# Kernel optimization log

Hardware: AMD Instinct MI355X
Metric: run time of the kernel (lower is better)

The kernel has to match this reference:

```python
import jax, jax.numpy as jnp
import numpy as np

N_EMBD = 768
NUM_EXPERTS = 64
EXPERT_WIDTH = 256            # all experts uniform width (expert_sizes=[(64,256)])
TOTAL_WIDTH = NUM_EXPERTS * EXPERT_WIDTH  # 16384
TOP_K = 8


def setup_inputs() -> dict:
    key = jax.random.key(0)
    k1, k2, k3, k4 = jax.random.split(key, 4)
    B, S = 1, 2048
    x = jax.random.normal(k1, (B, S, N_EMBD), dtype=jnp.float32)
    # router: nn.Linear(n_embd, num_experts, bias=False) -> weight [E, n_embd]
    router_w = jax.random.normal(k2, (NUM_EXPERTS, N_EMBD), dtype=jnp.float32) * 0.02
    # trunc_normal(std=0.02) approximated by clipped normal
    w1 = jnp.clip(jax.random.normal(k3, (N_EMBD, TOTAL_WIDTH), dtype=jnp.float32) * 0.02, -0.06, 0.06)
    w2 = jnp.clip(jax.random.normal(k4, (TOTAL_WIDTH, N_EMBD), dtype=jnp.float32) * 0.02, -0.06, 0.06)
    return {"x": x, "router_w": router_w, "w1": w1, "w2": w2}


def reference(x, router_w, w1, w2):
    B, S, D = x.shape
    T = B * S
    x_flat = x.reshape(T, D)

    # Router: sigmoid gating + top-k
    router_logits = x_flat @ router_w.T                      # [T, E]
    router_probs = jax.nn.sigmoid(router_logits.astype(jnp.float32))
    top_k_weights, selected_experts = jax.lax.top_k(router_probs, TOP_K)  # [T, K]
    top_k_weights = top_k_weights / (top_k_weights.sum(axis=-1, keepdims=True) + 1e-20)
    top_k_weights = top_k_weights.astype(x.dtype)

    # Per-token expert combine weights [T, E]: 0 for unselected experts.
    tok_idx = jnp.arange(T)[:, None]
    w_tok = jnp.zeros((T, NUM_EXPERTS), dtype=x.dtype).at[tok_idx, selected_experts].set(top_k_weights)

    # Expert MLP (relu^2 activation), dense-masked equivalent of
    # padded_gather -> grouped GEMM -> padded_scatter.
    h = jnp.square(jax.nn.relu(x_flat @ w1))                 # [T, E*W]
    h = (h.reshape(T, NUM_EXPERTS, EXPERT_WIDTH) * w_tok[:, :, None]).reshape(T, TOTAL_WIDTH)
    output = (h @ w2).reshape(B, S, D)

    # Aux losses
    router_z_loss = jnp.mean(jnp.square(jax.nn.logsumexp(router_logits, axis=-1)))
    tokens_per_expert = jnp.zeros((NUM_EXPERTS,), dtype=jnp.float32).at[selected_experts.reshape(-1)].add(1.0)
    f_i = (tokens_per_expert / tokens_per_expert.sum()).astype(x.dtype)
    p_i = router_probs.mean(axis=0)
    # all expert widths equal -> num_experts * (f_i . p_i)
    load_balance_loss = NUM_EXPERTS * (f_i.astype(jnp.float32) @ p_i)
    # expert_widths_normalized == ones -> mean over tokens of sum of probs
    compute_loss = router_probs.sum(axis=-1).mean()

    return output, router_z_loss, load_balance_loss, compute_loss, f_i
```

## Files before the change

### kernel.cpp

```cpp
#include <hip/hip_runtime.h>
#include <hip/hip_bf16.h>

#define T_TOKENS 2048
#define D_EMBD 768
#define N_EXP 64
#define EW 256
#define TOPK 8
#define TW (N_EXP*EW)
#define PAD_SLOTS 20480
#define SCHED_MAX 2560
#define OUT_BASE (2048*768)

typedef __attribute__((ext_vector_type(8))) short bf16x8;
typedef __attribute__((ext_vector_type(4))) float f32x4;

typedef __attribute__((address_space(1))) void GAS;
typedef __attribute__((address_space(3))) void LAS;
#define GLOAD16(g, l) __builtin_amdgcn_global_load_lds((GAS*)(g), (LAS*)(l), 16, 0, 0)

__device__ inline unsigned short f2bu(float f) {
  union { __hip_bfloat16 b; unsigned short u; } cv; cv.b = __float2bfloat16(f); return cv.u;
}
__device__ inline unsigned int pk2(float a, float b) {
  return (unsigned int)f2bu(a) | ((unsigned int)f2bu(b) << 16);
}

__global__ void k_init(int* counts, int* cursor, float* psum, float* scal,
                       float* wgt_slot, int* tok_slot, int* sched_e) {
  int i = blockIdx.x*256 + threadIdx.x;
  if (i < N_EXP) { counts[i] = 0; cursor[i] = 0; psum[i] = 0.f; }
  if (i < 2) scal[i] = 0.f;
  if (i < PAD_SLOTS) { wgt_slot[i] = 0.f; tok_slot[i] = 0; }
  if (i < SCHED_MAX) sched_e[i] = -1;
}

__global__ __launch_bounds__(256) void k_logits(const float* __restrict__ x,
                                                const float* __restrict__ rw,
                                                float* __restrict__ lp) {
  __shared__ float rw_s[8][256];
  int tid = threadIdx.x;
  int tg = blockIdx.x, eg = blockIdx.y, kc = blockIdx.z;
  #pragma unroll
  for (int idx = 0; idx < 8; idx++)
    rw_s[idx][tid] = rw[(size_t)(eg*8 + idx)*D_EMBD + kc*256 + tid];
  __syncthreads();
  int tok = tg*256 + tid;
  const float4* x4 = reinterpret_cast<const float4*>(x + (size_t)tok*D_EMBD + kc*256);
  float acc[8];
  #pragma unroll
  for (int e = 0; e < 8; e++) acc[e] = 0.f;
  #pragma unroll 4
  for (int k4 = 0; k4 < 64; k4++) {
    float4 xv = x4[k4];
    #pragma unroll
    for (int e = 0; e < 8; e++)
      acc[e] += xv.x*rw_s[e][k4*4+0] + xv.y*rw_s[e][k4*4+1]
              + xv.z*rw_s[e][k4*4+2] + xv.w*rw_s[e][k4*4+3];
  }
  float* dst = lp + (size_t)kc*T_TOKENS*N_EXP + (size_t)tok*N_EXP + eg*8;
  float4 o0 = {acc[0], acc[1], acc[2], acc[3]};
  float4 o1 = {acc[4], acc[5], acc[6], acc[7]};
  reinterpret_cast<float4*>(dst)[0] = o0;
  reinterpret_cast<float4*>(dst)[1] = o1;
}

__global__ __launch_bounds__(256) void k_router2(const float* __restrict__ lp,
                          int* __restrict__ sel_e, float* __restrict__ sel_w,
                          int* __restrict__ counts, float* __restrict__ psum,
                          float* __restrict__ scal) {
  __shared__ float psum_s[4][64];
  __shared__ int cnt_s[4][64];
  int tid = threadIdx.x, wv = tid >> 6, lane = tid & 63;
  float pacc = 0.f, zacc = 0.f;
  int cacc = 0;
  int tbase = blockIdx.x*8 + wv*2;
  #pragma unroll
  for (int it = 0; it < 2; it++) {
    int t = tbase + it;
    float logit = lp[(size_t)t*N_EXP + lane]
                + lp[(size_t)T_TOKENS*N_EXP + (size_t)t*N_EXP + lane]
                + lp[2*(size_t)T_TOKENS*N_EXP + (size_t)t*N_EXP + lane];
    float prob = 1.f/(1.f + expf(-logit));
    pacc += prob;
    float mx = logit;
    for (int s = 32; s; s >>= 1) mx = fmaxf(mx, __shfl_xor(mx, s, 64));
    float sse = expf(logit - mx);
    for (int s = 32; s; s >>= 1) sse += __shfl_xor(sse, s, 64);
    float lse = mx + logf(sse);
    zacc += lse*lse;
    int rank = 0;
    #pragma unroll
    for (int j = 0; j < 64; j++) {
      float pj = __shfl(prob, j, 64);
      rank += (pj > prob || (pj == prob && j < lane)) ? 1 : 0;
    }
    bool sel = rank < TOPK;
    float sp = sel ? prob : 0.f;
    for (int s = 32; s; s >>= 1) sp += __shfl_xor(sp, s, 64);
    if (sel) {
      sel_e[t*TOPK + rank] = lane;
      sel_w[t*TOPK + rank] = prob / (sp + 1e-20f);
      cacc++;
    }
  }
  psum_s[wv][lane] = pacc;
  cnt_s[wv][lane] = cacc;
  if (lane == 0) atomicAdd(&scal[0], zacc);
  __syncthreads();
  if (tid < 64) {
    float p = psum_s[0][tid] + psum_s[1][tid] + psum_s[2][tid] + psum_s[3][tid];
    int c = cnt_s[0][tid] + cnt_s[1][tid] + cnt_s[2][tid] + cnt_s[3][tid];
    atomicAdd(&psum[tid], p);
    atomicAdd(&counts[tid], c);
  }
}

__global__ void k_schedule(const int* __restrict__ counts, int* __restrict__ offsets,
                           int* __restrict__ sched_e, int* __restrict__ sched_r0) {
  int e = threadIdx.x;
  int c = counts[e];
  int tiles = (c + 63) >> 6;
  int padded = tiles << 6;
  int ip = padded;
  for (int s = 1; s < 64; s <<= 1) { int v = __shfl_up(ip, s, 64); if (e >= s) ip += v; }
  int rowoff = ip - padded;
  offsets[e] = rowoff;
  int it = tiles;
  for (int s = 8; s < 64; s <<= 1) { int v = __shfl_up(it, s, 64); if (e >= s) it += v; }
  int rank = it - tiles;
  int xcd = e & 7;
  for (int i = 0; i < tiles; i++) {
    int p = xcd + 8*(rank + i);
    sched_e[p] = e;
    sched_r0[p] = rowoff + i*64;
  }
}

__global__ void k_assign(const int* __restrict__ sel_e, const float* __restrict__ sel_w,
                         const int* __restrict__ offsets, int* __restrict__ cursor,
                         int* __restrict__ tok_slot, float* __restrict__ wgt_slot,
                         int* __restrict__ slot_tk) {
  int i = blockIdx.x*256 + threadIdx.x;
  int e = sel_e[i];
  int pos = atomicAdd(&cursor[e], 1);
  int slot = offsets[e] + pos;
  tok_slot[slot] = i >> 3;
  wgt_slot[slot] = sel_w[i];
  slot_tk[i] = slot;
}

template<int MODE>
__global__ __launch_bounds__(256) void k_moe_gemm(
    const void* __restrict__ Asrc, const float* __restrict__ Bsrc,
    const int* __restrict__ sched_e, const int* __restrict__ sched_r0,
    const int* __restrict__ tok_slot, const float* __restrict__ wgt_slot,
    __hip_bfloat16* __restrict__ outp) {
  constexpr int NS   = (MODE == 1) ? 12 : 4;
  constexpr int BSTR = (MODE == 1) ? TW : D_EMBD;
  __shared__ __hip_bfloat16 As[2][64*64];
  __shared__ __hip_bfloat16 Bs[2][128*64];
  int tid = threadIdx.x;
  int nch = blockIdx.y;
  int n4 = tid & 31, kpb = tid >> 5;
  int mrow = tid >> 4, k4f = tid & 15;
  int arl = tid >> 3, akc = tid & 7;
  int a_off = ((akc ^ (arl & 7)) << 3);
  int wv = tid >> 6, lane = tid & 63;
  int wm = wv >> 1, wn = wv & 1;
  int l15 = lane & 15, l4 = lane >> 4;

  for (int p = blockIdx.x; p < SCHED_MAX; p += gridDim.x) {
    int e = sched_e[p];
    if (e < 0) continue;
    int r0 = sched_r0[p];

    int browb = (MODE == 1) ? 0 : e*EW;
    int bcolb = (MODE == 1) ? (e*EW + nch*128) : nch*128;

    int tks[4];
    size_t a_base0 = 0, a_base1 = 0;
    if (MODE == 1) {
      #pragma unroll
      for (int i = 0; i < 4; i++) tks[i] = tok_slot[r0 + i*16 + mrow];
    } else {
      a_base0 = (size_t)(r0 + arl) * EW;
      a_base1 = (size_t)(r0 + arl + 32) * EW;
    }

    float bv[8][4], av[4][4];

    auto B_LOAD = [&](int k0) {
      const float* rp = Bsrc + (size_t)(browb + k0 + kpb*8)*BSTR + bcolb + n4*4;
      #pragma unroll
      for (int r = 0; r < 8; r++)
        *reinterpret_cast<float4*>(&bv[r][0]) =
            *reinterpret_cast<const float4*>(rp + (size_t)r*BSTR);
    };
    auto B_WRITE = [&](int bsel) {
      char* bs = (char*)&Bs[bsel][0];
      #pragma unroll
      for (int c = 0; c < 4; c++) {
        int n = n4*4 + c;
        int ch = kpb ^ ((n & 7) ^ ((n >> 3) & 7));
        uint4 o = { pk2(bv[0][c], bv[1][c]), pk2(bv[2][c], bv[3][c]),
                    pk2(bv[4][c], bv[5][c]), pk2(bv[6][c], bv[7][c]) };
        *reinterpret_cast<uint4*>(bs + n*128 + ch*16) = o;
      }
    };
    auto A_LOAD1 = [&](int k0) {
      const float* xf = (const float*)Asrc;
      #pragma unroll
      for (int i = 0; i < 4; i++)
        *reinterpret_cast<float4*>(&av[i][0]) =
            *reinterpret_cast<const float4*>(xf + (size_t)tks[i]*D_EMBD + k0 + k4f*4);
    };
    auto A_WRITE1 = [&](int bsel) {
      char* as_ = (char*)&As[bsel][0];
      #pragma unroll
      for (int i = 0; i < 4; i++) {
        int m = i*16 + mrow;
        int ch = (k4f >> 1) ^ (m & 7);
        uint2 val = { pk2(av[i][0], av[i][1]), pk2(av[i][2], av[i][3]) };
        *reinterpret_cast<uint2*>(as_ + m*128 + ch*16 + (k4f & 1)*8) = val;
      }
    };
    auto A_GLOAD2 = [&](int bsel, int k0) {
      const __hip_bfloat16* hb = (const __hip_bfloat16*)Asrc;
      GLOAD16(hb + a_base0 + k0 + a_off, &As[bsel][0] + tid*8);
      GLOAD16(hb + a_base1 + k0 + a_off, &As[bsel][0] + (256 + tid)*8);
    };

    f32x4 acc[2][4];
    f32x4 z = {0.f, 0.f, 0.f, 0.f};
    #pragma unroll
    for (int m = 0; m < 2; m++)
      #pragma unroll
      for (int n = 0; n < 4; n++) acc[m][n] = z;

    if (MODE == 1) { A_LOAD1(0); B_LOAD(0); A_WRITE1(0); B_WRITE(0); }
    else           { A_GLOAD2(0, 0); B_LOAD(0); B_WRITE(0);
                     asm volatile("s_waitcnt vmcnt(0)" ::: "memory"); }
    __syncthreads();

    int cur = 0;
    for (int step = 0; step < NS; step++) {
      bool more = (step + 1 < NS);
      int k1 = (step + 1)*64;
      if (more) {
        if (MODE == 1) { A_LOAD1(k1); B_LOAD(k1); }
        else           { A_GLOAD2(cur ^ 1, k1); B_LOAD(k1); }
      }
      const char* asC = (const char*)&As[cur][0];
      const char* bsC = (const char*)&Bs[cur][0];
      bf16x8 af[2][2], bq[4][2];
      #pragma unroll
      for (int m = 0; m < 2; m++) {
        int ra = wm*32 + m*16 + l15;
        #pragma unroll
        for (int kk = 0; kk < 2; kk++)
          af[m][kk] = *reinterpret_cast<const bf16x8*>(
              asC + ra*128 + (((kk*4 + l4) ^ (ra & 7)) << 4));
      }
      #pragma unroll
      for (int n = 0; n < 4; n++) {
        int rb = wn*64 + n*16 + l15;
        int Sb = (rb & 7) ^ ((rb >> 3) & 7);
        #pragma unroll
        for (int kk = 0; kk < 2; kk++)
          bq[n][kk] = *reinterpret_cast<const bf16x8*>(
              bsC + rb*128 + (((kk*4 + l4) ^ Sb) << 4));
      }
      #pragma unroll
      for (int kk = 0; kk < 2; kk++)
        #pragma unroll
        for (int m = 0; m < 2; m++)
          #pragma unroll
          for (int n = 0; n < 4; n++)
            acc[m][n] = __builtin_amdgcn_mfma_f32_16x16x32_bf16(af[m][kk], bq[n][kk], acc[m][n], 0, 0, 0);
      if (more) {
        if (MODE == 1) { A_WRITE1(cur ^ 1); B_WRITE(cur ^ 1); }
        else           { B_WRITE(cur ^ 1);
                         asm volatile("s_waitcnt vmcnt(0)" ::: "memory"); }
      }
      __syncthreads();
      cur ^= 1;
    }

    if (MODE == 1) {
      #pragma unroll
      for (int m = 0; m < 2; m++)
        #pragma unroll
        for (int j = 0; j < 4; j++) {
          int r = r0 + wm*32 + m*16 + l4*4 + j;
          float wg = wgt_slot[r];
          #pragma unroll
          for (int n = 0; n < 4; n++) {
            int col = nch*128 + wn*64 + n*16 + l15;
            float v = fmaxf(acc[m][n][j], 0.f);
            outp[(size_t)r*EW + col] = __float2bfloat16(v*v*wg);
          }
        }
    } else {
      #pragma unroll
      for (int m = 0; m < 2; m++)
        #pragma unroll
        for (int j = 0; j < 4; j++) {
          int r = r0 + wm*32 + m*16 + l4*4 + j;
          #pragma unroll
          for (int n = 0; n < 4; n++) {
            int col = nch*128 + wn*64 + n*16 + l15;
            outp[(size_t)r*D_EMBD + col] = __float2bfloat16(acc[m][n][j]);
          }
        }
    }
  }
}

__global__ void k_combine(const __hip_bfloat16* __restrict__ y, const int* __restrict__ slot_tk,
                          float* __restrict__ out) {
  __shared__ int s[TOPK];
  int t = blockIdx.x, tid = threadIdx.x;
  if (tid < TOPK) s[tid] = slot_tk[t*TOPK + tid];
  __syncthreads();
  if (tid < 192) {
    int c = tid*4;
    float a0 = 0.f, a1 = 0.f, a2 = 0.f, a3 = 0.f;
    #pragma unroll
    for (int k = 0; k < TOPK; k++) {
      ushort4 v = *reinterpret_cast<const ushort4*>(&y[(size_t)s[k]*D_EMBD + c]);
      union { unsigned int u; float f; } f0, f1, f2, f3;
      f0.u = ((unsigned int)v.x) << 16;
      f1.u = ((unsigned int)v.y) << 16;
      f2.u = ((unsigned int)v.z) << 16;
      f3.u = ((unsigned int)v.w) << 16;
      a0 += f0.f; a1 += f1.f; a2 += f2.f; a3 += f3.f;
    }
    float4 o = {a0, a1, a2, a3};
    *reinterpret_cast<float4*>(&out[(size_t)t*D_EMBD + c]) = o;
  }
}

__global__ void k_finalize(const int* __restrict__ counts, const float* __restrict__ psum,
                           const float* __restrict__ scal, float* __restrict__ out) {
  __shared__ float part[N_EXP], ptot[N_EXP];
  int e = threadIdx.x;
  float f = (float)counts[e] / 16384.f;
  float p = psum[e] / 2048.f;
  part[e] = f * p;
  ptot[e] = p;
  out[OUT_BASE + 3 + e] = f;
  __syncthreads();
  if (e == 0) {
    float s = 0.f, q = 0.f;
    for (int i = 0; i < N_EXP; i++) { s += part[i]; q += ptot[i]; }
    out[OUT_BASE + 0] = scal[0] / 2048.f;
    out[OUT_BASE + 1] = 64.f * s;
    out[OUT_BASE + 2] = q;
  }
}

extern "C" void kernel_launch(void* const* d_in, const int* in_sizes, int n_in,
                              void* d_out, int out_size, void* d_ws, size_t ws_size,
                              hipStream_t stream) {
  const float* x  = (const float*)d_in[0];
  const float* rw = (const float*)d_in[1];
  const float* w1 = (const float*)d_in[2];
  const float* w2 = (const float*)d_in[3];
  float* out = (float*)d_out;
  char* ws = (char*)d_ws;

  size_t o = 0;
  auto alloc = [&](size_t b) { size_t r = o; o += (b + 255) & ~(size_t)255; return r; };
  __hip_bfloat16* hprm  = (__hip_bfloat16*)(ws + alloc((size_t)PAD_SLOTS*256*2));
  __hip_bfloat16* yprm  = (__hip_bfloat16*)(ws + alloc((size_t)PAD_SLOTS*768*2));
  float* lp      = (float*)(ws + alloc(3UL*2048*64*4));
  int*   sel_e   = (int*)  (ws + alloc(16384UL*4));
  float* sel_w   = (float*)(ws + alloc(16384UL*4));
  int*   slot_tk = (int*)  (ws + alloc(16384UL*4));
  int*   tokslot = (int*)  (ws + alloc((size_t)PAD_SLOTS*4));
  float* wgtslot = (float*)(ws + alloc((size_t)PAD_SLOTS*4));
  int*   counts  = (int*)  (ws + alloc(256));
  int*   cursor  = (int*)  (ws + alloc(256));
  float* psum    = (float*)(ws + alloc(256));
  float* scal    = (float*)(ws + alloc(256));
  int*   offsets = (int*)  (ws + alloc(256));
  int*   sch_e   = (int*)  (ws + alloc(SCHED_MAX*4));
  int*   sch_r0  = (int*)  (ws + alloc(SCHED_MAX*4));

  k_init<<<80, 256, 0, stream>>>(counts, cursor, psum, scal, wgtslot, tokslot, sch_e);
  k_logits<<<dim3(8, 8, 3), 256, 0, stream>>>(x, rw, lp);
  k_router2<<<256, 256, 0, stream>>>(lp, sel_e, sel_w, counts, psum, scal);
  k_schedule<<<1, 64, 0, stream>>>(counts, offsets, sch_e, sch_r0);
  k_assign<<<64, 256, 0, stream>>>(sel_e, sel_w, offsets, cursor, tokslot, wgtslot, slot_tk);
  k_moe_gemm<1><<<dim3(512, 2), 256, 0, stream>>>((const void*)x, w1, sch_e, sch_r0, tokslot, wgtslot, hprm);
  k_moe_gemm<2><<<dim3(512, 6), 256, 0, stream>>>((const void*)hprm, w2, sch_e, sch_r0, tokslot, wgtslot, yprm);
  k_combine<<<2048, 256, 0, stream>>>(yprm, slot_tk, out);
  k_finalize<<<1, 64, 0, stream>>>(counts, psum, scal, out);
}
```

Before: 141.7 us.

## Fuse expert up- and down-projection GEMMs into one kernel with LDS-resident hidden tile

Merges the two MoE GEMM kernels into one. Each block computes the 64x256 relu²-weighted hidden tile for its row group into shared memory, then immediately multiplies it by the expert's w2 slice for all six output column chunks. This removes the bf16 hidden buffer round-trip through global memory and one kernel launch. In exchange, per-block parallelism drops from 8 blocks per schedule entry (2+6 via grid y) to one block doing all the work. LDS use also grows by 32KB, which lowers occupancy and serializes the work inside each block.

```diff
diff --git a/kernel.cpp b/kernel.cpp
--- a/kernel.cpp
+++ b/kernel.cpp
@@ -13,10 +13,6 @@
 
 typedef __attribute__((ext_vector_type(8))) short bf16x8;
 typedef __attribute__((ext_vector_type(4))) float f32x4;
-
-typedef __attribute__((address_space(1))) void GAS;
-typedef __attribute__((address_space(3))) void LAS;
-#define GLOAD16(g, l) __builtin_amdgcn_global_load_lds((GAS*)(g), (LAS*)(l), 16, 0, 0)
 
 __device__ inline unsigned short f2bu(float f) {
   union { __hip_bfloat16 b; unsigned short u; } cv; cv.b = __float2bfloat16(f); return cv.u;
@@ -149,22 +145,18 @@
   slot_tk[i] = slot;
 }
 
-template<int MODE>
-__global__ __launch_bounds__(256) void k_moe_gemm(
-    const void* __restrict__ Asrc, const float* __restrict__ Bsrc,
+__global__ __launch_bounds__(256) void k_moe_mlp(
+    const float* __restrict__ x, const float* __restrict__ w1,
+    const float* __restrict__ w2,
     const int* __restrict__ sched_e, const int* __restrict__ sched_r0,
     const int* __restrict__ tok_slot, const float* __restrict__ wgt_slot,
-    __hip_bfloat16* __restrict__ outp) {
-  constexpr int NS   = (MODE == 1) ? 12 : 4;
-  constexpr int BSTR = (MODE == 1) ? TW : D_EMBD;
+    __hip_bfloat16* __restrict__ yprm) {
   __shared__ __hip_bfloat16 As[2][64*64];
   __shared__ __hip_bfloat16 Bs[2][128*64];
+  __shared__ __hip_bfloat16 Hs[64*256];
   int tid = threadIdx.x;
-  int nch = blockIdx.y;
   int n4 = tid & 31, kpb = tid >> 5;
   int mrow = tid >> 4, k4f = tid & 15;
-  int arl = tid >> 3, akc = tid & 7;
-  int a_off = ((akc ^ (arl & 7)) << 3);
   int wv = tid >> 6, lane = tid & 63;
   int wm = wv >> 1, wn = wv & 1;
   int l15 = lane & 15, l4 = lane >> 4;
@@ -174,29 +166,27 @@
     if (e < 0) continue;
     int r0 = sched_r0[p];
 
-    int browb = (MODE == 1) ? 0 : e*EW;
-    int bcolb = (MODE == 1) ? (e*EW + nch*128) : nch*128;
-
     int tks[4];
-    size_t a_base0 = 0, a_base1 = 0;
-    if (MODE == 1) {
-      #pragma unroll
-      for (int i = 0; i < 4; i++) tks[i] = tok_slot[r0 + i*16 + mrow];
-    } else {
-      a_base0 = (size_t)(r0 + arl) * EW;
-      a_base1 = (size_t)(r0 + arl + 32) * EW;
-    }
+    #pragma unroll
+    for (int i = 0; i < 4; i++) tks[i] = tok_slot[r0 + i*16 + mrow];
+
+    const float* bsrc = w1;
+    int bstr = TW;
+    size_t browb = 0;
+    int bcolb = 0;
 
     float bv[8][4], av[4][4];
-
-    auto B_LOAD = [&](int k0) {
-      const float* rp = Bsrc + (size_t)(browb + k0 + kpb*8)*BSTR + bcolb + n4*4;
+    f32x4 acc[2][4];
+    f32x4 z = {0.f, 0.f, 0.f, 0.f};
+
+    auto B_LD = [&](int k0) {
+      const float* rp = bsrc + (browb + (size_t)(k0 + kpb*8))*bstr + bcolb + n4*4;
       #pragma unroll
       for (int r = 0; r < 8; r++)
         *reinterpret_cast<float4*>(&bv[r][0]) =
-            *reinterpret_cast<const float4*>(rp + (size_t)r*BSTR);
-    };
-    auto B_WRITE = [&](int bsel) {
+            *reinterpret_cast<const float4*>(rp + (size_t)r*bstr);
+    };
+    auto B_WR = [&](int bsel) {
       char* bs = (char*)&Bs[bsel][0];
       #pragma unroll
       for (int c = 0; c < 4; c++) {
@@ -207,14 +197,13 @@
         *reinterpret_cast<uint4*>(bs + n*128 + ch*16) = o;
       }
     };
-    auto A_LOAD1 = [&](int k0) {
-      const float* xf = (const float*)Asrc;
+    auto A_LD = [&](int k0) {
       #pragma unroll
       for (int i = 0; i < 4; i++)
         *reinterpret_cast<float4*>(&av[i][0]) =
-            *reinterpret_cast<const float4*>(xf + (size_t)tks[i]*D_EMBD + k0 + k4f*4);
-    };
-    auto A_WRITE1 = [&](int bsel) {
+            *reinterpret_cast<const float4*>(x + (size_t)tks[i]*D_EMBD + k0 + k4f*4);
+    };
+    auto A_WR = [&](int bsel) {
       char* as_ = (char*)&As[bsel][0];
       #pragma unroll
       for (int i = 0; i < 4; i++) {
@@ -224,43 +213,14 @@
         *reinterpret_cast<uint2*>(as_ + m*128 + ch*16 + (k4f & 1)*8) = val;
       }
     };
-    auto A_GLOAD2 = [&](int bsel, int k0) {
-      const __hip_bfloat16* hb = (const __hip_bfloat16*)Asrc;
-      GLOAD16(hb + a_base0 + k0 + a_off, &As[bsel][0] + tid*8);
-      GLOAD16(hb + a_base1 + k0 + a_off, &As[bsel][0] + (256 + tid)*8);
-    };
-
-    f32x4 acc[2][4];
-    f32x4 z = {0.f, 0.f, 0.f, 0.f};
-    #pragma unroll
-    for (int m = 0; m < 2; m++)
-      #pragma unroll
-      for (int n = 0; n < 4; n++) acc[m][n] = z;
-
-    if (MODE == 1) { A_LOAD1(0); B_LOAD(0); A_WRITE1(0); B_WRITE(0); }
-    else           { A_GLOAD2(0, 0); B_LOAD(0); B_WRITE(0);
-                     asm volatile("s_waitcnt vmcnt(0)" ::: "memory"); }
-    __syncthreads();
-
-    int cur = 0;
-    for (int step = 0; step < NS; step++) {
-      bool more = (step + 1 < NS);
-      int k1 = (step + 1)*64;
-      if (more) {
-        if (MODE == 1) { A_LOAD1(k1); B_LOAD(k1); }
-        else           { A_GLOAD2(cur ^ 1, k1); B_LOAD(k1); }
-      }
-      const char* asC = (const char*)&As[cur][0];
-      const char* bsC = (const char*)&Bs[cur][0];
-      bf16x8 af[2][2], bq[4][2];
-      #pragma unroll
-      for (int m = 0; m < 2; m++) {
-        int ra = wm*32 + m*16 + l15;
-        #pragma unroll
-        for (int kk = 0; kk < 2; kk++)
-          af[m][kk] = *reinterpret_cast<const bf16x8*>(
-              asC + ra*128 + (((kk*4 + l4) ^ (ra & 7)) << 4));
-      }
+    auto ZERO = [&]() {
+      #pragma unroll
+      for (int m = 0; m < 2; m++)
+        #pragma unroll
+        for (int n = 0; n < 4; n++) acc[m][n] = z;
+    };
+    auto MFMA_AB = [&](bf16x8 (&af)[2][2], const char* bsC) {
+      bf16x8 bq[4][2];
       #pragma unroll
       for (int n = 0; n < 4; n++) {
         int rb = wn*64 + n*16 + l15;
@@ -277,30 +237,80 @@
           #pragma unroll
           for (int n = 0; n < 4; n++)
             acc[m][n] = __builtin_amdgcn_mfma_f32_16x16x32_bf16(af[m][kk], bq[n][kk], acc[m][n], 0, 0, 0);
-      if (more) {
-        if (MODE == 1) { A_WRITE1(cur ^ 1); B_WRITE(cur ^ 1); }
-        else           { B_WRITE(cur ^ 1);
-                         asm volatile("s_waitcnt vmcnt(0)" ::: "memory"); }
+    };
+
+    #pragma unroll 1
+    for (int nch1 = 0; nch1 < 2; nch1++) {
+      bsrc = w1; bstr = TW; browb = 0; bcolb = e*EW + nch1*128;
+      ZERO();
+      A_LD(0); B_LD(0); A_WR(0); B_WR(0);
+      __syncthreads();
+      int cur = 0;
+      for (int step = 0; step < 12; step++) {
+        bool more = (step + 1 < 12);
+        if (more) { A_LD((step + 1)*64); B_LD((step + 1)*64); }
+        const char* asC = (const char*)&As[cur][0];
+        bf16x8 af[2][2];
+        #pragma unroll
+        for (int m = 0; m < 2; m++) {
+          int ra = wm*32 + m*16 + l15;
+          #pragma unroll
+          for (int kk = 0; kk < 2; kk++)
+            af[m][kk] = *reinterpret_cast<const bf16x8*>(
+                asC + ra*128 + (((kk*4 + l4) ^ (ra & 7)) << 4));
+        }
+        MFMA_AB(af, (const char*)&Bs[cur][0]);
+        if (more) { A_WR(cur ^ 1); B_WR(cur ^ 1); }
+        __syncthreads();
+        cur ^= 1;
       }
-      __syncthreads();
-      cur ^= 1;
-    }
-
-    if (MODE == 1) {
+      char* hsC = (char*)&Hs[0];
       #pragma unroll
       for (int m = 0; m < 2; m++)
         #pragma unroll
         for (int j = 0; j < 4; j++) {
-          int r = r0 + wm*32 + m*16 + l4*4 + j;
-          float wg = wgt_slot[r];
+          int row = wm*32 + m*16 + l4*4 + j;
+          float wg = wgt_slot[r0 + row];
           #pragma unroll
           for (int n = 0; n < 4; n++) {
-            int col = nch*128 + wn*64 + n*16 + l15;
+            int col = nch1*128 + wn*64 + n*16 + l15;
             float v = fmaxf(acc[m][n][j], 0.f);
-            outp[(size_t)r*EW + col] = __float2bfloat16(v*v*wg);
+            int g = col >> 3;
+            int ch = (g & ~7) | ((g & 7) ^ (row & 7));
+            *reinterpret_cast<unsigned short*>(hsC + row*512 + ch*16 + (col & 7)*2)
+                = f2bu(v*v*wg);
           }
         }
-    } else {
+    }
+    __syncthreads();
+
+    const char* hsC = (const char*)&Hs[0];
+    #pragma unroll 1
+    for (int nch = 0; nch < 6; nch++) {
+      bsrc = w2; bstr = D_EMBD; browb = (size_t)e*EW; bcolb = nch*128;
+      ZERO();
+      B_LD(0); B_WR(0);
+      __syncthreads();
+      int cur = 0;
+      for (int step = 0; step < 4; step++) {
+        bool more = (step + 1 < 4);
+        if (more) B_LD((step + 1)*64);
+        bf16x8 af[2][2];
+        #pragma unroll
+        for (int m = 0; m < 2; m++) {
+          int ra = wm*32 + m*16 + l15;
+          #pragma unroll
+          for (int kk = 0; kk < 2; kk++) {
+            int g = step*8 + kk*4 + l4;
+            int ch = (g & ~7) | ((g & 7) ^ (ra & 7));
+            af[m][kk] = *reinterpret_cast<const bf16x8*>(hsC + ra*512 + ch*16);
+          }
+        }
+        MFMA_AB(af, (const char*)&Bs[cur][0]);
+        if (more) B_WR(cur ^ 1);
+        __syncthreads();
+        cur ^= 1;
+      }
       #pragma unroll
       for (int m = 0; m < 2; m++)
         #pragma unroll
@@ -309,10 +319,11 @@
           #pragma unroll
           for (int n = 0; n < 4; n++) {
             int col = nch*128 + wn*64 + n*16 + l15;
-            outp[(size_t)r*D_EMBD + col] = __float2bfloat16(acc[m][n][j]);
+            yprm[(size_t)r*D_EMBD + col] = __float2bfloat16(acc[m][n][j]);
           }
         }
     }
+    __syncthreads();
   }
 }
 
@@ -371,7 +382,6 @@
 
   size_t o = 0;
   auto alloc = [&](size_t b) { size_t r = o; o += (b + 255) & ~(size_t)255; return r; };
-  __hip_bfloat16* hprm  = (__hip_bfloat16*)(ws + alloc((size_t)PAD_SLOTS*256*2));
   __hip_bfloat16* yprm  = (__hip_bfloat16*)(ws + alloc((size_t)PAD_SLOTS*768*2));
   float* lp      = (float*)(ws + alloc(3UL*2048*64*4));
   int*   sel_e   = (int*)  (ws + alloc(16384UL*4));
@@ -392,8 +402,7 @@
   k_router2<<<256, 256, 0, stream>>>(lp, sel_e, sel_w, counts, psum, scal);
   k_schedule<<<1, 64, 0, stream>>>(counts, offsets, sch_e, sch_r0);
   k_assign<<<64, 256, 0, stream>>>(sel_e, sel_w, offsets, cursor, tokslot, wgtslot, slot_tk);
-  k_moe_gemm<1><<<dim3(512, 2), 256, 0, stream>>>((const void*)x, w1, sch_e, sch_r0, tokslot, wgtslot, hprm);
-  k_moe_gemm<2><<<dim3(512, 6), 256, 0, stream>>>((const void*)hprm, w2, sch_e, sch_r0, tokslot, wgtslot, yprm);
+  k_moe_mlp<<<512, 256, 0, stream>>>(x, w1, w2, sch_e, sch_r0, tokslot, wgtslot, yprm);
   k_combine<<<2048, 256, 0, stream>>>(yprm, slot_tk, out);
   k_finalize<<<1, 64, 0, stream>>>(counts, psum, scal, out);
 }
```

New measurement: 152.1 us. 7.4% more time.

## Widen MoE GEMM tiles to 64x256 with 512-thread blocks and register-staged A loads

Applied to the files above, without the earlier changes.

Doubles the expert GEMM block to 512 threads and the N tile from 128 to 256 columns, so each 64-row token tile is gathered and converted once per full expert width instead of twice (or six times for the down projection). The A-tile async global-to-LDS loads are replaced with register-staged loads and swizzled LDS writes, and the compute loop is restructured into 8 waves each handling 16 rows by 128 columns. This cuts redundant A-gather and f32 weight-read traffic but halves the block count per schedule entry, raises LDS use, and loses the direct-to-LDS load path.

```diff
diff --git a/kernel.cpp b/kernel.cpp
--- a/kernel.cpp
+++ b/kernel.cpp
@@ -13,10 +13,6 @@
 
 typedef __attribute__((ext_vector_type(8))) short bf16x8;
 typedef __attribute__((ext_vector_type(4))) float f32x4;
-
-typedef __attribute__((address_space(1))) void GAS;
-typedef __attribute__((address_space(3))) void LAS;
-#define GLOAD16(g, l) __builtin_amdgcn_global_load_lds((GAS*)(g), (LAS*)(l), 16, 0, 0)
 
 __device__ inline unsigned short f2bu(float f) {
   union { __hip_bfloat16 b; unsigned short u; } cv; cv.b = __float2bfloat16(f); return cv.u;
@@ -150,7 +146,7 @@
 }
 
 template<int MODE>
-__global__ __launch_bounds__(256) void k_moe_gemm(
+__global__ __launch_bounds__(512) void k_moe_gemm(
     const void* __restrict__ Asrc, const float* __restrict__ Bsrc,
     const int* __restrict__ sched_e, const int* __restrict__ sched_r0,
     const int* __restrict__ tok_slot, const float* __restrict__ wgt_slot,
@@ -158,13 +154,11 @@
   constexpr int NS   = (MODE == 1) ? 12 : 4;
   constexpr int BSTR = (MODE == 1) ? TW : D_EMBD;
   __shared__ __hip_bfloat16 As[2][64*64];
-  __shared__ __hip_bfloat16 Bs[2][128*64];
+  __shared__ __hip_bfloat16 Bs[2][256*64];
   int tid = threadIdx.x;
   int nch = blockIdx.y;
-  int n4 = tid & 31, kpb = tid >> 5;
-  int mrow = tid >> 4, k4f = tid & 15;
-  int arl = tid >> 3, akc = tid & 7;
-  int a_off = ((akc ^ (arl & 7)) << 3);
+  int n4 = tid & 63, kpb = tid >> 6;
+  int arow = tid >> 3, akc = tid & 7;
   int wv = tid >> 6, lane = tid & 63;
   int wm = wv >> 1, wn = wv & 1;
   int l15 = lane & 15, l4 = lane >> 4;
@@ -174,29 +168,26 @@
     if (e < 0) continue;
     int r0 = sched_r0[p];
 
-    int browb = (MODE == 1) ? 0 : e*EW;
-    int bcolb = (MODE == 1) ? (e*EW + nch*128) : nch*128;
-
-    int tks[4];
-    size_t a_base0 = 0, a_base1 = 0;
-    if (MODE == 1) {
-      #pragma unroll
-      for (int i = 0; i < 4; i++) tks[i] = tok_slot[r0 + i*16 + mrow];
-    } else {
-      a_base0 = (size_t)(r0 + arl) * EW;
-      a_base1 = (size_t)(r0 + arl + 32) * EW;
-    }
-
-    float bv[8][4], av[4][4];
-
-    auto B_LOAD = [&](int k0) {
-      const float* rp = Bsrc + (size_t)(browb + k0 + kpb*8)*BSTR + bcolb + n4*4;
+    size_t browb = (MODE == 1) ? 0 : (size_t)e*EW;
+    int bcolb = (MODE == 1) ? e*EW : nch*EW;
+
+    int tok = 0;
+    size_t a_base = 0;
+    if (MODE == 1) tok = tok_slot[r0 + arow];
+    else           a_base = (size_t)(r0 + arow) * EW;
+
+    float bv[8][4];
+    float av[8];
+    uint4 au;
+
+    auto B_LD = [&](int k0) {
+      const float* rp = Bsrc + (browb + (size_t)(k0 + kpb*8))*BSTR + bcolb + n4*4;
       #pragma unroll
       for (int r = 0; r < 8; r++)
         *reinterpret_cast<float4*>(&bv[r][0]) =
             *reinterpret_cast<const float4*>(rp + (size_t)r*BSTR);
     };
-    auto B_WRITE = [&](int bsel) {
+    auto B_WR = [&](int bsel) {
       char* bs = (char*)&Bs[bsel][0];
       #pragma unroll
       for (int c = 0; c < 4; c++) {
@@ -207,39 +198,56 @@
         *reinterpret_cast<uint4*>(bs + n*128 + ch*16) = o;
       }
     };
-    auto A_LOAD1 = [&](int k0) {
+    auto A_LD1 = [&](int k0) {
       const float* xf = (const float*)Asrc;
-      #pragma unroll
-      for (int i = 0; i < 4; i++)
-        *reinterpret_cast<float4*>(&av[i][0]) =
-            *reinterpret_cast<const float4*>(xf + (size_t)tks[i]*D_EMBD + k0 + k4f*4);
-    };
-    auto A_WRITE1 = [&](int bsel) {
+      const float4* rp = reinterpret_cast<const float4*>(xf + (size_t)tok*D_EMBD + k0 + akc*8);
+      *reinterpret_cast<float4*>(&av[0]) = rp[0];
+      *reinterpret_cast<float4*>(&av[4]) = rp[1];
+    };
+    auto A_WR1 = [&](int bsel) {
       char* as_ = (char*)&As[bsel][0];
-      #pragma unroll
-      for (int i = 0; i < 4; i++) {
-        int m = i*16 + mrow;
-        int ch = (k4f >> 1) ^ (m & 7);
-        uint2 val = { pk2(av[i][0], av[i][1]), pk2(av[i][2], av[i][3]) };
-        *reinterpret_cast<uint2*>(as_ + m*128 + ch*16 + (k4f & 1)*8) = val;
-      }
-    };
-    auto A_GLOAD2 = [&](int bsel, int k0) {
+      int ch = akc ^ (arow & 7);
+      uint4 o = { pk2(av[0], av[1]), pk2(av[2], av[3]),
+                  pk2(av[4], av[5]), pk2(av[6], av[7]) };
+      *reinterpret_cast<uint4*>(as_ + arow*128 + ch*16) = o;
+    };
+    auto A_LD2 = [&](int k0) {
       const __hip_bfloat16* hb = (const __hip_bfloat16*)Asrc;
-      GLOAD16(hb + a_base0 + k0 + a_off, &As[bsel][0] + tid*8);
-      GLOAD16(hb + a_base1 + k0 + a_off, &As[bsel][0] + (256 + tid)*8);
-    };
-
-    f32x4 acc[2][4];
+      au = *reinterpret_cast<const uint4*>(hb + a_base + k0 + (akc ^ (arow & 7))*8);
+    };
+    auto A_WR2 = [&](int bsel) {
+      char* as_ = (char*)&As[bsel][0];
+      *reinterpret_cast<uint4*>(as_ + arow*128 + (akc ^ (arow & 7))*16) = au;
+    };
+
+    f32x4 acc[8];
     f32x4 z = {0.f, 0.f, 0.f, 0.f};
     #pragma unroll
-    for (int m = 0; m < 2; m++)
-      #pragma unroll
-      for (int n = 0; n < 4; n++) acc[m][n] = z;
-
-    if (MODE == 1) { A_LOAD1(0); B_LOAD(0); A_WRITE1(0); B_WRITE(0); }
-    else           { A_GLOAD2(0, 0); B_LOAD(0); B_WRITE(0);
-                     asm volatile("s_waitcnt vmcnt(0)" ::: "memory"); }
+    for (int n = 0; n < 8; n++) acc[n] = z;
+
+    auto COMPUTE = [&](int bsel) {
+      const char* asC = (const char*)&As[bsel][0];
+      const char* bsC = (const char*)&Bs[bsel][0];
+      int ra = wm*16 + l15;
+      bf16x8 af0 = *reinterpret_cast<const bf16x8*>(
+          asC + ra*128 + (((0*4 + l4) ^ (ra & 7)) << 4));
+      bf16x8 af1 = *reinterpret_cast<const bf16x8*>(
+          asC + ra*128 + (((1*4 + l4) ^ (ra & 7)) << 4));
+      #pragma unroll
+      for (int n = 0; n < 8; n++) {
+        int rb = wn*128 + n*16 + l15;
+        int Sb = (rb & 7) ^ ((rb >> 3) & 7);
+        bf16x8 b0 = *reinterpret_cast<const bf16x8*>(
+            bsC + rb*128 + (((0*4 + l4) ^ Sb) << 4));
+        bf16x8 b1 = *reinterpret_cast<const bf16x8*>(
+            bsC + rb*128 + (((1*4 + l4) ^ Sb) << 4));
+        acc[n] = __builtin_amdgcn_mfma_f32_16x16x32_bf16(af0, b0, acc[n], 0, 0, 0);
+        acc[n] = __builtin_amdgcn_mfma_f32_16x16x32_bf16(af1, b1, acc[n], 0, 0, 0);
+      }
+    };
+
+    if (MODE == 1) { A_LD1(0); B_LD(0); A_WR1(0); B_WR(0); }
+    else           { A_LD2(0); B_LD(0); A_WR2(0); B_WR(0); }
     __syncthreads();
 
     int cur = 0;
@@ -247,40 +255,13 @@
       bool more = (step + 1 < NS);
       int k1 = (step + 1)*64;
       if (more) {
-        if (MODE == 1) { A_LOAD1(k1); B_LOAD(k1); }
-        else           { A_GLOAD2(cur ^ 1, k1); B_LOAD(k1); }
-      }
-      const char* asC = (const char*)&As[cur][0];
-      const char* bsC = (const char*)&Bs[cur][0];
-      bf16x8 af[2][2], bq[4][2];
-      #pragma unroll
-      for (int m = 0; m < 2; m++) {
-        int ra = wm*32 + m*16 + l15;
-        #pragma unroll
-        for (int kk = 0; kk < 2; kk++)
-          af[m][kk] = *reinterpret_cast<const bf16x8*>(
-              asC + ra*128 + (((kk*4 + l4) ^ (ra & 7)) << 4));
-      }
-      #pragma unroll
-      for (int n = 0; n < 4; n++) {
-        int rb = wn*64 + n*16 + l15;
-        int Sb = (rb & 7) ^ ((rb >> 3) & 7);
-        #pragma unroll
-        for (int kk = 0; kk < 2; kk++)
-          bq[n][kk] = *reinterpret_cast<const bf16x8*>(
-              bsC + rb*128 + (((kk*4 + l4) ^ Sb) << 4));
-      }
-      #pragma unroll
-      for (int kk = 0; kk < 2; kk++)
-        #pragma unroll
-        for (int m = 0; m < 2; m++)
-          #pragma unroll
-          for (int n = 0; n < 4; n++)
-            acc[m][n] = __builtin_amdgcn_mfma_f32_16x16x32_bf16(af[m][kk], bq[n][kk], acc[m][n], 0, 0, 0);
+        if (MODE == 1) { A_LD1(k1); B_LD(k1); }
+        else           { A_LD2(k1); B_LD(k1); }
+      }
+      COMPUTE(cur);
       if (more) {
-        if (MODE == 1) { A_WRITE1(cur ^ 1); B_WRITE(cur ^ 1); }
-        else           { B_WRITE(cur ^ 1);
-                         asm volatile("s_waitcnt vmcnt(0)" ::: "memory"); }
+        if (MODE == 1) { A_WR1(cur ^ 1); B_WR(cur ^ 1); }
+        else           { A_WR2(cur ^ 1); B_WR(cur ^ 1); }
       }
       __syncthreads();
       cur ^= 1;
@@ -288,30 +269,26 @@
 
     if (MODE == 1) {
       #pragma unroll
-      for (int m = 0; m < 2; m++)
+      for (int j = 0; j < 4; j++) {
+        int r = r0 + wm*16 + l4*4 + j;
+        float wg = wgt_slot[r];
         #pragma unroll
-        for (int j = 0; j < 4; j++) {
-          int r = r0 + wm*32 + m*16 + l4*4 + j;
-          float wg = wgt_slot[r];
-          #pragma unroll
-          for (int n = 0; n < 4; n++) {
-            int col = nch*128 + wn*64 + n*16 + l15;
-            float v = fmaxf(acc[m][n][j], 0.f);
-            outp[(size_t)r*EW + col] = __float2bfloat16(v*v*wg);
-          }
+        for (int n = 0; n < 8; n++) {
+          int col = wn*128 + n*16 + l15;
+          float v = fmaxf(acc[n][j], 0.f);
+          outp[(size_t)r*EW + col] = __float2bfloat16(v*v*wg);
         }
+      }
     } else {
       #pragma unroll
-      for (int m = 0; m < 2; m++)
+      for (int j = 0; j < 4; j++) {
+        int r = r0 + wm*16 + l4*4 + j;
         #pragma unroll
-        for (int j = 0; j < 4; j++) {
-          int r = r0 + wm*32 + m*16 + l4*4 + j;
-          #pragma unroll
-          for (int n = 0; n < 4; n++) {
-            int col = nch*128 + wn*64 + n*16 + l15;
-            outp[(size_t)r*D_EMBD + col] = __float2bfloat16(acc[m][n][j]);
-          }
+        for (int n = 0; n < 8; n++) {
+          int col = nch*EW + wn*128 + n*16 + l15;
+          outp[(size_t)r*D_EMBD + col] = __float2bfloat16(acc[n][j]);
         }
+      }
     }
   }
 }
@@ -392,8 +369,8 @@
   k_router2<<<256, 256, 0, stream>>>(lp, sel_e, sel_w, counts, psum, scal);
   k_schedule<<<1, 64, 0, stream>>>(counts, offsets, sch_e, sch_r0);
   k_assign<<<64, 256, 0, stream>>>(sel_e, sel_w, offsets, cursor, tokslot, wgtslot, slot_tk);
-  k_moe_gemm<1><<<dim3(512, 2), 256, 0, stream>>>((const void*)x, w1, sch_e, sch_r0, tokslot, wgtslot, hprm);
-  k_moe_gemm<2><<<dim3(512, 6), 256, 0, stream>>>((const void*)hprm, w2, sch_e, sch_r0, tokslot, wgtslot, yprm);
+  k_moe_gemm<1><<<dim3(512, 1), 512, 0, stream>>>((const void*)x, w1, sch_e, sch_r0, tokslot, wgtslot, hprm);
+  k_moe_gemm<2><<<dim3(512, 3), 512, 0, stream>>>((const void*)hprm, w2, sch_e, sch_r0, tokslot, wgtslot, yprm);
   k_combine<<<2048, 256, 0, stream>>>(yprm, slot_tk, out);
   k_finalize<<<1, 64, 0, stream>>>(counts, psum, scal, out);
 }
```

Measured after the change: 149.4 us. +5.5%, slower.
